# Kernel optimization log

Hardware: AMD Instinct MI355X
Metric: run time of the kernel (lower is better)

## Reference

```python
import jax, jax.numpy as jnp
import numpy as np

HEADS = 8
DIM_HEAD = 64
HIDDEN = HEADS * DIM_HEAD  # 512
Q_DIM = 320
KV_DIM = 640


def setup_inputs() -> dict:
    key = jax.random.key(0)
    k1, k2, k3, k4, k5 = jax.random.split(key, 5)
    x_q = jax.random.normal(k1, (8, Q_DIM, 32, 32), dtype=jnp.float32)
    x_kv = jax.random.normal(k2, (8, KV_DIM, 32, 32), dtype=jnp.float32)
    # conv1x1 weights stored as [out_channels, in_channels]
    w_q = jax.random.normal(k3, (HIDDEN, Q_DIM), dtype=jnp.float32) * (Q_DIM ** -0.5)
    w_kv = jax.random.normal(k4, (2 * HIDDEN, KV_DIM), dtype=jnp.float32) * (KV_DIM ** -0.5)
    w_out = jax.random.normal(k5, (Q_DIM, HIDDEN), dtype=jnp.float32) * (HIDDEN ** -0.5)
    return {"x_q": x_q, "x_kv": x_kv, "w_q": w_q, "w_kv": w_kv, "w_out": w_out}


def reference(x_q, x_kv, w_q, w_kv, w_out):
    b, c, h, w = x_q.shape
    scale = DIM_HEAD ** -0.5
    n = h * w
    # 1x1 conv == channel matmul
    q = jnp.einsum('oc,bcxy->boxy', w_q, x_q).reshape(b, HEADS, DIM_HEAD, n) * scale
    kv = jnp.einsum('oc,bcxy->boxy', w_kv, x_kv)
    k_, v_ = jnp.split(kv, 2, axis=1)
    k_ = k_.reshape(b, HEADS, DIM_HEAD, n)
    v_ = v_.reshape(b, HEADS, DIM_HEAD, n)
    sim = jnp.einsum('bhdi,bhdj->bhij', q, k_)
    sim = sim - jax.lax.stop_gradient(sim.max(axis=-1, keepdims=True))
    attn = jax.nn.softmax(sim, axis=-1)
    out = jnp.einsum('bhij,bhdj->bhid', attn, v_)  # [b,h,n,d]
    out = out.transpose(0, 1, 3, 2).reshape(b, HIDDEN, h, w)  # 'b h (x y) d -> b (h d) x y'
    return jnp.einsum('oc,bcxy->boxy', w_out, out)
```

## Files before the change

### kernel.cpp

```cpp
#include <hip/hip_runtime.h>
#include <math.h>

#define BB   8
#define HH   8
#define DDIM 64
#define NN   1024
#define HID  512
#define COUT 320

typedef float4 f4;
typedef __bf16 bf16;
typedef __attribute__((ext_vector_type(8))) __bf16 bf16x8;
typedef __attribute__((ext_vector_type(4))) __bf16 bf16x4;
typedef __attribute__((ext_vector_type(4))) float f32x4;

#define MFMA16(a,b,c) __builtin_amdgcn_mfma_f32_16x16x32_bf16((a),(b),(c),0,0,0)

__device__ __forceinline__ void gll16(const bf16* g, char* l) {
    __builtin_amdgcn_global_load_lds(
        (const __attribute__((address_space(1))) void*)g,
        (__attribute__((address_space(3))) void*)l, 16, 0, 0);
}

template<int CIN>
__device__ __forceinline__
void conv_w_body(const float* __restrict__ W, bf16* __restrict__ Wh,
                 bf16* __restrict__ Wl, int rows_valid, int bx)
{
    const int idx = bx * 256 + threadIdx.x;
    const int row = idx / (CIN / 4);
    const int c4  = (idx % (CIN / 4)) * 4;
    f4 v = {0.f, 0.f, 0.f, 0.f};
    if (row < rows_valid) v = *(const f4*)&W[(size_t)row * CIN + c4];
    const float vv[4] = {v.x, v.y, v.z, v.w};
    bf16x4 hv, lv;
#pragma unroll
    for (int e = 0; e < 4; ++e) {
        bf16 hb = (bf16)vv[e];
        hv[e] = hb;
        lv[e] = (bf16)(vv[e] - (float)hb);
    }
    *(bf16x4*)&Wh[(size_t)row * CIN + c4] = hv;
    if (Wl) *(bf16x4*)&Wl[(size_t)row * CIN + c4] = lv;
}

template<int CIN>
__device__ __forceinline__
void conv_xt_body(const float* __restrict__ X, bf16* __restrict__ Xt,
                  float (*Xs)[68], int bx, int by, int bz)
{
    const int n0 = bx * 64;
    const int c0 = by * 64;
    const int t  = threadIdx.x;
    const float* Xb = X + (size_t)bz * CIN * NN;
#pragma unroll
    for (int it = 0; it < 4; ++it) {
        const int r  = it * 16 + (t >> 4);
        const int cc = (t & 15) * 4;
        *(f4*)&Xs[r][cc] = *(const f4*)&Xb[(size_t)(c0 + r) * NN + n0 + cc];
    }
    __syncthreads();
    const int n  = t >> 2;
    const int cb = (t & 3) * 16;
    union { bf16 h[16]; uint4 u[2]; } o;
#pragma unroll
    for (int e = 0; e < 16; ++e) o.h[e] = (bf16)Xs[cb + e][n];
    bf16* dst = Xt + ((size_t)bz * NN + n0 + n) * CIN + c0 + cb;
    *(uint4*)dst = o.u[0];
    *(uint4*)(dst + 8) = o.u[1];
}

__global__ __launch_bounds__(256)
void prep_kernel(const float* __restrict__ x_q, const float* __restrict__ x_kv,
                 const float* __restrict__ w_q, const float* __restrict__ w_kv,
                 const float* __restrict__ w_out,
                 bf16* __restrict__ Xtq, bf16* __restrict__ Xtkv,
                 bf16* __restrict__ Wqh,
                 bf16* __restrict__ Wkvh,
                 bf16* __restrict__ Wouth, bf16* __restrict__ Woutl)
{
    __shared__ __align__(16) float Xs[64][68];
    const int id = blockIdx.x;
    if (id < 640) {
        const int r = id >> 4;
        conv_xt_body<320>(x_q, Xtq, Xs, id & 15, r % 5, r / 5);
    } else if (id < 1920) {
        const int i = id - 640, r = i >> 4;
        conv_xt_body<640>(x_kv, Xtkv, Xs, i & 15, r % 10, r / 10);
    } else if (id < 2080) {
        conv_w_body<320>(w_q, Wqh, nullptr, 512, id - 1920);
    } else if (id < 2720) {
        conv_w_body<640>(w_kv, Wkvh, nullptr, 1024, id - 2080);
    } else {
        conv_w_body<512>(w_out, Wouth, Woutl, 320, id - 2720);
    }
}

template<int K, int TERMS, int ASPLIT, int EPI>
__device__ __forceinline__
void gemm_body(char* lds,
               const bf16* __restrict__ Ah, const bf16* __restrict__ Al,
               const bf16* __restrict__ Bh, const bf16* __restrict__ Bl,
               long a_bstride, long b_bstride,
               bf16* __restrict__ D0,
               float* __restrict__ Df, float scale,
               int bx, int by, int bz)
{
    constexpr int BUFB = (TERMS == 2) ? 24576 : 16384;
    constexpr int BOFF = (TERMS == 2) ? 16384 : 8192;

    const int t  = threadIdx.x;
    const int w  = t >> 6, l = t & 63;
    const int lg = l >> 4, lq = l & 15;
    const int wa = w >> 1, wb = w & 1;
    const int arow0 = by * 128;
    const int brow0 = bx * 128;

    const bf16* Ab = Ah + (size_t)bz * a_bstride;
    const bf16* Bb = Bh + (size_t)bz * b_bstride;

    const int srow = 16 * w + (l >> 2);
    const int cw   = (l & 3) ^ ((l >> 3) & 3);
    const bf16* pA = Ab + (size_t)(arow0 + srow) * K + cw * 8;
    const bf16* pB = Bb + (size_t)(brow0 + srow) * K + cw * 8;
    const bf16* pX = nullptr;
    if constexpr (TERMS == 2) {
        const bf16* Xb = ASPLIT ? (Al + (size_t)bz * a_bstride)
                                : (Bl + (size_t)bz * b_bstride);
        pX = Xb + (size_t)((ASPLIT ? arow0 : brow0) + srow) * K + cw * 8;
    }
    const int woff = w * 1024;

    f32x4 acc[4][4];
#pragma unroll
    for (int i = 0; i < 4; ++i)
#pragma unroll
        for (int j = 0; j < 4; ++j) acc[i][j] = (f32x4){0.f, 0.f, 0.f, 0.f};

    constexpr int NK = K / 32;

    auto issue = [&](int ks2, int pbuf) {
        char* Bd = lds + pbuf * BUFB + woff;
        const int ko = ks2 * 32;
        gll16(pA + ko,          Bd);
        gll16(pA + 64 * K + ko, Bd + 4096);
        if constexpr (TERMS == 2) {
            gll16(pX + ko,          Bd + 8192);
            gll16(pX + 64 * K + ko, Bd + 8192 + 4096);
        }
        gll16(pB + ko,          Bd + BOFF);
        gll16(pB + 64 * K + ko, Bd + BOFF + 4096);
    };

    issue(0, 0);

    for (int ks = 0; ks < NK; ++ks) {
        const int p = ks & 1;
        if (ks + 1 < NK) {
            issue(ks + 1, p ^ 1);
            if constexpr (TERMS == 2)
                asm volatile("s_waitcnt vmcnt(6)" ::: "memory");
            else
                asm volatile("s_waitcnt vmcnt(4)" ::: "memory");
        } else {
            asm volatile("s_waitcnt vmcnt(0)" ::: "memory");
        }
        __builtin_amdgcn_s_barrier();
        __builtin_amdgcn_sched_barrier(0);

        char* buf = lds + p * BUFB;
        bf16x8 a0[4], a1[4], b0[4], b1[4];
#pragma unroll
        for (int m = 0; m < 4; ++m) {
            const int rA = wa * 64 + 16 * m + lq;
            const int offA = rA * 64 + ((lg ^ ((rA >> 1) & 3)) << 4);
            a0[m] = *(const bf16x8*)(buf + offA);
            if (TERMS == 2 && ASPLIT) a1[m] = *(const bf16x8*)(buf + 8192 + offA);
            const int rB = wb * 64 + 16 * m + lq;
            const int offB = rB * 64 + ((lg ^ ((rB >> 1) & 3)) << 4);
            b0[m] = *(const bf16x8*)(buf + BOFF + offB);
            if (TERMS == 2 && !ASPLIT) b1[m] = *(const bf16x8*)(buf + 8192 + offB);
        }
        __builtin_amdgcn_s_setprio(1);
#pragma unroll
        for (int mA = 0; mA < 4; ++mA)
#pragma unroll
            for (int mB = 0; mB < 4; ++mB) {
                acc[mA][mB] = MFMA16(a0[mA], b0[mB], acc[mA][mB]);
                if constexpr (TERMS == 2) {
                    acc[mA][mB] = ASPLIT ? MFMA16(a1[mA], b0[mB], acc[mA][mB])
                                         : MFMA16(a0[mA], b1[mB], acc[mA][mB]);
                }
            }
        __builtin_amdgcn_s_setprio(0);
        asm volatile("s_waitcnt lgkmcnt(0)" ::: "memory");
        __builtin_amdgcn_s_barrier();
        __builtin_amdgcn_sched_barrier(0);
    }

#pragma unroll
    for (int mA = 0; mA < 4; ++mA)
#pragma unroll
        for (int mB = 0; mB < 4; ++mB) {
            if (EPI == 4) {
                const int o = arow0 + wa * 64 + 16 * mA + 4 * lg;
                const int i = brow0 + wb * 64 + 16 * mB + lq;
                const int h = o >> 6, d = o & 63;
                const size_t base = ((size_t)((bz * HH + h) * NN + i)) * 64 + d;
                bf16x4 hv;
#pragma unroll
                for (int r = 0; r < 4; ++r) hv[r] = (bf16)(acc[mA][mB][r] * scale);
                *(bf16x4*)(D0 + base) = hv;
            } else if (EPI == 2) {
                const int i = arow0 + wa * 64 + 16 * mA + 4 * lg;
                const int o = brow0 + wb * 64 + 16 * mB + lq;
                const int h = o >> 6, d = o & 63;
                const size_t base = ((size_t)((bz * HH + h) * DDIM + d)) * NN + i;
                bf16x4 pv;
#pragma unroll
                for (int r = 0; r < 4; ++r) pv[r] = (bf16)acc[mA][mB][r];
                *(bf16x4*)(D0 + base) = pv;
            } else {
                const int i = arow0 + wa * 64 + 16 * mA + 4 * lg;
                const int o = brow0 + wb * 64 + 16 * mB + lq;
                if (o < COUT)
                    *(f32x4*)(Df + ((size_t)(bz * COUT + o)) * NN + i) = acc[mA][mB];
            }
        }
}

#define QSCALE (0.125f * 1.44269504f)

__global__ __launch_bounds__(256, 4)
void gemm_qkv_kernel(const bf16* __restrict__ Xtq, const bf16* __restrict__ Xtkv,
                     const bf16* __restrict__ Wqh, const bf16* __restrict__ Wkvh,
                     bf16* __restrict__ Qhi, bf16* __restrict__ Khi,
                     bf16* __restrict__ Vt)
{
    __shared__ __align__(16) char lds[32768];
    const int id = blockIdx.x;
    if (id < 256) {
        gemm_body<320, 1, 0, 4>(lds, Wqh, nullptr, Xtq, nullptr, 0, (long)NN * 320,
                                Qhi, nullptr, QSCALE,
                                id & 7, (id >> 3) & 3, id >> 5);
    } else if (id < 512) {
        const int i = id - 256;
        gemm_body<640, 1, 0, 4>(lds, Wkvh, nullptr, Xtkv, nullptr, 0, (long)NN * 640,
                                Khi, nullptr, 1.0f,
                                i & 7, (i >> 3) & 3, i >> 5);
    } else {
        const int i = id - 512;
        gemm_body<640, 1, 0, 2>(lds, Xtkv, nullptr,
                                Wkvh + (size_t)HID * 640, nullptr,
                                (long)NN * 640, 0, Vt, nullptr, 1.0f,
                                i & 3, (i >> 2) & 7, i >> 5);
    }
}

__global__ __launch_bounds__(256, 2)
void outproj_kernel(const bf16* __restrict__ Ot,
                    const bf16* __restrict__ Wouth, const bf16* __restrict__ Woutl,
                    float* __restrict__ out)
{
    __shared__ __align__(16) char lds[49152];
    gemm_body<512, 2, 0, 3>(lds, Ot, nullptr, Wouth, Woutl, (long)NN * HID, 0,
                            nullptr, out, 1.0f,
                            blockIdx.x, blockIdx.y, blockIdx.z);
}

__global__ __launch_bounds__(256, 5)
void attn_kernel(const bf16* __restrict__ Qhi, const bf16* __restrict__ Khi,
                 const bf16* __restrict__ Vt, bf16* __restrict__ Ot)
{
    const int id  = blockIdx.x;
    const int loc = id >> 3;
    const int bh  = (id & 7) * 8 + (loc >> 4);
    const int i0  = (loc & 15) * 64;
    const int b   = bh >> 3, h = bh & 7;
    const int t   = threadIdx.x;
    const int w   = t >> 6;
    const int l   = t & 63;
    const int lg  = l >> 4;
    const int lq  = l & 15;

    __shared__ __align__(16) char lds[32768];

    const size_t qbase = ((size_t)(bh * NN) + i0 + w * 16 + lq) * DDIM + lg * 8;
    bf16x8 qh[2];
    qh[0] = *(const bf16x8*)(Qhi + qbase);
    qh[1] = *(const bf16x8*)(Qhi + qbase + 32);

    const int l8 = l >> 3;
    const int cw = (l & 7) ^ l8;
    const bf16* KhS = Khi + ((size_t)(bh * NN) + 16 * w + l8) * DDIM + cw * 8;
    const bf16* VS  = Vt  + (((size_t)(bh * DDIM) + 16 * w + l8) << 10) + cw * 8;
    char* const Lw = lds + (w << 11);

    f32x4 Oa[4];
#pragma unroll
    for (int m = 0; m < 4; ++m) { Oa[m][0]=0.f; Oa[m][1]=0.f; Oa[m][2]=0.f; Oa[m][3]=0.f; }
    float l_lane = 0.f;

    {
        gll16(KhS,        Lw);
        gll16(KhS + 512,  Lw + 1024);
        gll16(VS,         Lw + 8192);
        gll16(VS + 8192,  Lw + 8192 + 1024);
    }

    for (int jt = 0; jt < 16; ++jt) {
        const int p = jt & 1;
        if (jt < 15) {
            char* B = Lw + 16384 * (p ^ 1);
            const bf16* kh = KhS + ((jt + 1) << 12);
            const bf16* vs = VS + ((jt + 1) << 6);
            gll16(kh,        B);
            gll16(kh + 512,  B + 1024);
            gll16(vs,        B + 8192);
            gll16(vs + 8192, B + 8192 + 1024);
            asm volatile("s_waitcnt vmcnt(4)" ::: "memory");
        } else {
            asm volatile("s_waitcnt vmcnt(0)" ::: "memory");
        }
        __builtin_amdgcn_s_barrier();
        __builtin_amdgcn_sched_barrier(0);

        char* buf = lds + 16384 * p;
        char* Pw  = buf + (w << 11);

        f32x4 S[4];
        __builtin_amdgcn_s_setprio(1);
#pragma unroll
        for (int m = 0; m < 4; ++m) {
            f32x4 acc = {0.f, 0.f, 0.f, 0.f};
#pragma unroll
            for (int ks = 0; ks < 2; ++ks) {
                const int row = lq + 16 * m;
                const int ch  = ((lg + 4 * ks) ^ (row & 7)) << 4;
                bf16x8 kh = *(const bf16x8*)(buf + row * 128 + ch);
                acc = MFMA16(kh, qh[ks], acc);
            }
            S[m] = acc;
        }
        __builtin_amdgcn_s_setprio(0);

        float ps[4][4];
#pragma unroll
        for (int m = 0; m < 4; ++m)
#pragma unroll
            for (int r = 0; r < 4; ++r) {
                const float p2 = __builtin_exp2f(S[m][r]);
                ps[m][r] = p2;
                l_lane += p2;
            }

        __builtin_amdgcn_s_barrier();

#pragma unroll
        for (int f = 0; f < 4; ++f) {
            union { bf16 hh[4]; uint2 u; } pu;
            pu.hh[0] = (bf16)ps[f][0];
            pu.hh[1] = (bf16)ps[f][1];
            pu.hh[2] = (bf16)ps[f][2];
            pu.hh[3] = (bf16)ps[f][3];
            *(uint2*)(Pw + lq * 128 + (((2 * f + (lg >> 1)) ^ (lq & 7)) << 4) + ((lg & 1) << 3)) = pu.u;
        }

#pragma unroll
        for (int ks = 0; ks < 2; ++ks) {
            bf16x8 pb = *(const bf16x8*)(Pw + lq * 128 + (((lg + 4 * ks) ^ (lq & 7)) << 4));
            __builtin_amdgcn_s_setprio(1);
#pragma unroll
            for (int m = 0; m < 4; ++m) {
                const int row = lq + 16 * m;
                bf16x8 va = *(const bf16x8*)(buf + 8192 + row * 128 + (((lg + 4 * ks) ^ (row & 7)) << 4));
                Oa[m] = MFMA16(va, pb, Oa[m]);
            }
            __builtin_amdgcn_s_setprio(0);
        }

        asm volatile("s_waitcnt lgkmcnt(0)" ::: "memory");
        __builtin_amdgcn_s_barrier();
        __builtin_amdgcn_sched_barrier(0);
    }

    float l_run = l_lane;
    l_run += __shfl_xor(l_run, 16);
    l_run += __shfl_xor(l_run, 32);
    const float inv = 1.0f / l_run;
    const int i = i0 + w * 16 + lq;
    const size_t obase = ((size_t)(b * NN) + i) * HID + h * DDIM;
#pragma unroll
    for (int m = 0; m < 4; ++m) {
        bf16x4 ov;
#pragma unroll
        for (int r = 0; r < 4; ++r) ov[r] = (bf16)(Oa[m][r] * inv);
        *(bf16x4*)(Ot + obase + 16 * m + 4 * lg) = ov;
    }
}

extern "C" void kernel_launch(void* const* d_in, const int* in_sizes, int n_in,
                              void* d_out, int out_size, void* d_ws, size_t ws_size,
                              hipStream_t stream)
{
    const float* x_q   = (const float*)d_in[0];
    const float* x_kv  = (const float*)d_in[1];
    const float* w_q   = (const float*)d_in[2];
    const float* w_kv  = (const float*)d_in[3];
    const float* w_out = (const float*)d_in[4];
    float* out = (float*)d_out;

    char* ws = (char*)d_ws;
    bf16* Xtq   = (bf16*)(ws + 0);
    bf16* Ot    = (bf16*)(ws + 0);
    bf16* Xtkv  = (bf16*)(ws + 5242880);
    bf16* Wqh   = (bf16*)(ws + 15728640);
    bf16* Wkvh  = (bf16*)(ws + 16384000);
    bf16* Wouth = (bf16*)(ws + 19005440);
    bf16* Woutl = (bf16*)(ws + 19398656);
    bf16* Qhi   = (bf16*)(ws + 19791872);
    bf16* Khi   = (bf16*)(ws + 36569088);
    bf16* Vt    = (bf16*)(ws + 53346304);

    dim3 blk(256);
    prep_kernel<<<dim3(2912), blk, 0, stream>>>(x_q, x_kv, w_q, w_kv, w_out,
                                                Xtq, Xtkv, Wqh, Wkvh,
                                                Wouth, Woutl);
    gemm_qkv_kernel<<<dim3(768), blk, 0, stream>>>(Xtq, Xtkv, Wqh, Wkvh,
                                                   Qhi, Khi, Vt);
    attn_kernel<<<dim3(1024), blk, 0, stream>>>(Qhi, Khi, Vt, Ot);
    outproj_kernel<<<dim3(3, 8, 8), blk, 0, stream>>>(Ot, Wouth, Woutl, out);
}
```

Before: 85.89 us.

## Split attention key tiles across waves and keep P in registers

The attention kernel now splits each 64-key tile across its four waves, each wave taking 16 keys against all 64 queries, where before each wave owned 16 queries. Probabilities are fed straight from S into a 16x16x16 MFMA as the B operand via packed bf16 conversion. This removes the LDS round-trip for P and one mid-tile barrier. The cost is 64 accumulator registers per lane, which lowers the occupancy bound from 5 to 3. A final cross-wave reduction of the output and row sums through LDS float atomics is also added.

```diff
diff --git a/kernel.cpp b/kernel.cpp
--- a/kernel.cpp
+++ b/kernel.cpp
@@ -13,8 +13,10 @@
 typedef __attribute__((ext_vector_type(8))) __bf16 bf16x8;
 typedef __attribute__((ext_vector_type(4))) __bf16 bf16x4;
 typedef __attribute__((ext_vector_type(4))) float f32x4;
-
-#define MFMA16(a,b,c) __builtin_amdgcn_mfma_f32_16x16x32_bf16((a),(b),(c),0,0,0)
+typedef __attribute__((ext_vector_type(4))) short short4v;
+
+#define MFMA16(a,b,c)    __builtin_amdgcn_mfma_f32_16x16x32_bf16((a),(b),(c),0,0,0)
+#define MFMA16K16(a,b,c) __builtin_amdgcn_mfma_f32_16x16x16bf16_1k((a),(b),(c),0,0,0)
 
 __device__ __forceinline__ void gll16(const bf16* g, char* l) {
     __builtin_amdgcn_global_load_lds(
@@ -268,7 +270,7 @@
                             blockIdx.x, blockIdx.y, blockIdx.z);
 }
 
-__global__ __launch_bounds__(256, 5)
+__global__ __launch_bounds__(256, 3)
 void attn_kernel(const bf16* __restrict__ Qhi, const bf16* __restrict__ Khi,
                  const bf16* __restrict__ Vt, bf16* __restrict__ Ot)
 {
@@ -285,10 +287,13 @@
 
     __shared__ __align__(16) char lds[32768];
 
-    const size_t qbase = ((size_t)(bh * NN) + i0 + w * 16 + lq) * DDIM + lg * 8;
-    bf16x8 qh[2];
-    qh[0] = *(const bf16x8*)(Qhi + qbase);
-    qh[1] = *(const bf16x8*)(Qhi + qbase + 32);
+    bf16x8 qh[4][2];
+#pragma unroll
+    for (int qb = 0; qb < 4; ++qb)
+#pragma unroll
+        for (int ks = 0; ks < 2; ++ks)
+            qh[qb][ks] = *(const bf16x8*)(Qhi +
+                ((size_t)(bh * NN) + i0 + 16 * qb + lq) * DDIM + (lg + 4 * ks) * 8);
 
     const int l8 = l >> 3;
     const int cw = (l & 7) ^ l8;
@@ -296,10 +301,12 @@
     const bf16* VS  = Vt  + (((size_t)(bh * DDIM) + 16 * w + l8) << 10) + cw * 8;
     char* const Lw = lds + (w << 11);
 
-    f32x4 Oa[4];
-#pragma unroll
-    for (int m = 0; m < 4; ++m) { Oa[m][0]=0.f; Oa[m][1]=0.f; Oa[m][2]=0.f; Oa[m][3]=0.f; }
-    float l_lane = 0.f;
+    f32x4 Oa[4][4];
+#pragma unroll
+    for (int m = 0; m < 4; ++m)
+#pragma unroll
+        for (int qb = 0; qb < 4; ++qb) Oa[m][qb] = (f32x4){0.f, 0.f, 0.f, 0.f};
+    float l_lane[4] = {0.f, 0.f, 0.f, 0.f};
 
     {
         gll16(KhS,        Lw);
@@ -326,56 +333,39 @@
         __builtin_amdgcn_sched_barrier(0);
 
         char* buf = lds + 16384 * p;
-        char* Pw  = buf + (w << 11);
-
-        f32x4 S[4];
-        __builtin_amdgcn_s_setprio(1);
+
+        const int krow = 16 * w + lq;
+        const bf16x8 kf0 = *(const bf16x8*)(buf + krow * 128 + ((lg ^ (lq & 7)) << 4));
+        const bf16x8 kf1 = *(const bf16x8*)(buf + krow * 128 + (((4 + lg) ^ (lq & 7)) << 4));
+
+        short4v pb[4];
+#pragma unroll
+        for (int qb = 0; qb < 4; ++qb) {
+            f32x4 S = {0.f, 0.f, 0.f, 0.f};
+            __builtin_amdgcn_s_setprio(1);
+            S = MFMA16(kf0, qh[qb][0], S);
+            S = MFMA16(kf1, qh[qb][1], S);
+            __builtin_amdgcn_s_setprio(0);
+            const float p0 = __builtin_exp2f(S[0]);
+            const float p1 = __builtin_exp2f(S[1]);
+            const float p2 = __builtin_exp2f(S[2]);
+            const float p3 = __builtin_exp2f(S[3]);
+            l_lane[qb] += (p0 + p1) + (p2 + p3);
+            union { unsigned u[2]; short4v s; } pu;
+            asm("v_cvt_pk_bf16_f32 %0, %1, %2" : "=v"(pu.u[0]) : "v"(p0), "v"(p1));
+            asm("v_cvt_pk_bf16_f32 %0, %1, %2" : "=v"(pu.u[1]) : "v"(p2), "v"(p3));
+            pb[qb] = pu.s;
+        }
+
 #pragma unroll
         for (int m = 0; m < 4; ++m) {
-            f32x4 acc = {0.f, 0.f, 0.f, 0.f};
-#pragma unroll
-            for (int ks = 0; ks < 2; ++ks) {
-                const int row = lq + 16 * m;
-                const int ch  = ((lg + 4 * ks) ^ (row & 7)) << 4;
-                bf16x8 kh = *(const bf16x8*)(buf + row * 128 + ch);
-                acc = MFMA16(kh, qh[ks], acc);
-            }
-            S[m] = acc;
-        }
-        __builtin_amdgcn_s_setprio(0);
-
-        float ps[4][4];
-#pragma unroll
-        for (int m = 0; m < 4; ++m)
-#pragma unroll
-            for (int r = 0; r < 4; ++r) {
-                const float p2 = __builtin_exp2f(S[m][r]);
-                ps[m][r] = p2;
-                l_lane += p2;
-            }
-
-        __builtin_amdgcn_s_barrier();
-
-#pragma unroll
-        for (int f = 0; f < 4; ++f) {
-            union { bf16 hh[4]; uint2 u; } pu;
-            pu.hh[0] = (bf16)ps[f][0];
-            pu.hh[1] = (bf16)ps[f][1];
-            pu.hh[2] = (bf16)ps[f][2];
-            pu.hh[3] = (bf16)ps[f][3];
-            *(uint2*)(Pw + lq * 128 + (((2 * f + (lg >> 1)) ^ (lq & 7)) << 4) + ((lg & 1) << 3)) = pu.u;
-        }
-
-#pragma unroll
-        for (int ks = 0; ks < 2; ++ks) {
-            bf16x8 pb = *(const bf16x8*)(Pw + lq * 128 + (((lg + 4 * ks) ^ (lq & 7)) << 4));
+            const int vrow = 16 * m + lq;
+            const short4v va = *(const short4v*)(buf + 8192 + vrow * 128
+                + (((2 * w + (lg >> 1)) ^ (lq & 7)) << 4) + ((lg & 1) << 3));
             __builtin_amdgcn_s_setprio(1);
 #pragma unroll
-            for (int m = 0; m < 4; ++m) {
-                const int row = lq + 16 * m;
-                bf16x8 va = *(const bf16x8*)(buf + 8192 + row * 128 + (((lg + 4 * ks) ^ (row & 7)) << 4));
-                Oa[m] = MFMA16(va, pb, Oa[m]);
-            }
+            for (int qb = 0; qb < 4; ++qb)
+                Oa[m][qb] = MFMA16K16(va, pb[qb], Oa[m][qb]);
             __builtin_amdgcn_s_setprio(0);
         }
 
@@ -384,17 +374,42 @@
         __builtin_amdgcn_sched_barrier(0);
     }
 
-    float l_run = l_lane;
-    l_run += __shfl_xor(l_run, 16);
-    l_run += __shfl_xor(l_run, 32);
-    const float inv = 1.0f / l_run;
-    const int i = i0 + w * 16 + lq;
-    const size_t obase = ((size_t)(b * NN) + i) * HID + h * DDIM;
+    float* Og = (float*)lds;
+    float* Ls = (float*)(lds + 16384);
+    for (int z = t; z < 4096 + 64; z += 256) Og[z] = 0.f;
+    __syncthreads();
+
+#pragma unroll
+    for (int m = 0; m < 4; ++m)
+#pragma unroll
+        for (int qb = 0; qb < 4; ++qb)
+#pragma unroll
+            for (int r = 0; r < 4; ++r) {
+                const int d = 16 * m + 4 * lg + r;
+                const int q = 16 * qb + lq;
+                atomicAdd(&Og[d * 64 + (((q >> 2) ^ (d & 7)) << 2) + (q & 3)],
+                          Oa[m][qb][r]);
+            }
+#pragma unroll
+    for (int qb = 0; qb < 4; ++qb) {
+        float v = l_lane[qb];
+        v += __shfl_xor(v, 16);
+        v += __shfl_xor(v, 32);
+        if (lg == 0) atomicAdd(&Ls[16 * qb + lq], v);
+    }
+    __syncthreads();
+
+    const int qv = 16 * w + lq;
+    const float inv = 1.0f / Ls[qv];
+    const size_t obase = ((size_t)(b * NN) + i0 + qv) * HID + h * DDIM;
 #pragma unroll
     for (int m = 0; m < 4; ++m) {
         bf16x4 ov;
 #pragma unroll
-        for (int r = 0; r < 4; ++r) ov[r] = (bf16)(Oa[m][r] * inv);
+        for (int r = 0; r < 4; ++r) {
+            const int d = 16 * m + 4 * lg + r;
+            ov[r] = (bf16)(Og[d * 64 + (((qv >> 2) ^ (d & 7)) << 2) + (qv & 3)] * inv);
+        }
         *(bf16x4*)(Ot + obase + 16 * m + 4 * lg) = ov;
     }
 }
```

New measurement: 170.5 us. 1.98x slower.
